# Performance work log

Measured on AMD Instinct MI355X. Metric: run time of the kernel, lower is better.

The kernel has to match this reference:

```python
import jax, jax.numpy as jnp
import numpy as np
import math, itertools

RANGE = 1.0
DIM = 3
N_LEVELS = 16
N_FEATS = 2
HASHMAP_SIZE = 2 ** 15
BASE_RES = 16
FINEST_RES = 512
_b = math.exp((math.log(FINEST_RES) - math.log(BASE_RES)) / (N_LEVELS - 1))
RESOLUTIONS = [int(math.floor(BASE_RES * (_b ** i))) for i in range(N_LEVELS)]
PRIMES = np.array([1, 2654435761, 805459861], dtype=np.uint32)
# True -> take the lower corner (xi) along that dim, weight (1 - xf)
BIN_MASK = np.array(list(itertools.product([1, 0], repeat=DIM)), dtype=bool)  # (8, 3)


def setup_inputs() -> dict:
    key = jax.random.key(0)
    kx, kt = jax.random.split(key)
    x = jax.random.uniform(kx, (1048576, DIM), jnp.float32, minval=-RANGE, maxval=RANGE)
    # per-level hash tables (nn.Embedding weights), stacked: (L, 2^15, F)
    tables = jax.random.normal(kt, (N_LEVELS, HASHMAP_SIZE, N_FEATS), jnp.float32) * 0.01
    return {"x": x, "tables": tables}


def _encode_level(x01, table, res):
    # x01: (N, 3) in [0, 1];  table: (2^15, F)
    xs = x01 * res
    xi_f = jnp.floor(xs)
    xf = (xs - xi_f)[:, None, :]                       # (N, 1, 3) fractional part
    xi = xi_f.astype(jnp.uint32)[:, None, :]           # (N, 1, 3)
    mask = jnp.asarray(BIN_MASK)[None]                 # (1, 8, 3)
    corners = jnp.where(mask, xi, xi + jnp.uint32(1))  # (N, 8, 3)
    ws = jnp.prod(jnp.where(mask, 1.0 - xf, xf), axis=-1)  # (N, 8) trilinear weights
    h = corners * jnp.asarray(PRIMES)                  # uint32 mul with wraparound
    idx = (h[..., 0] ^ h[..., 1] ^ h[..., 2]) % jnp.uint32(HASHMAP_SIZE)  # (N, 8)
    feats = table[idx]                                 # (N, 8, F) irregular gather
    return jnp.sum(feats * ws[..., None], axis=-2)     # (N, F)


def reference(x, tables):
    # HashGridLoRAEncoder.forward: normalize to [0,1], encode, concat levels
    x01 = (x + RANGE) / (2.0 * RANGE)                  # (N, 3)
    outs = [_encode_level(x01, tables[i], RESOLUTIONS[i]) for i in range(N_LEVELS)]
    return jnp.concatenate(outs, axis=-1)              # (N, 32)
```

## Files before the change

### kernel.cpp

```cpp
#include <hip/hip_runtime.h>

#define TMASK 32767u
#define P2 2654435761u
#define P3 805459861u

typedef float f32x4 __attribute__((ext_vector_type(4)));
typedef unsigned u32x4 __attribute__((ext_vector_type(4)));

constexpr int NBINS = 32768;
constexpr int BLOCK = 128;
constexpr int HP = 17;

constexpr size_t WS_HIST   = 0;
constexpr size_t WS_CURSOR = 128 * 1024;
constexpr size_t WS_SORTED = 256 * 1024;
constexpr size_t WS_NEEDED = WS_SORTED + (size_t)1048576 * 16;

__device__ __forceinline__ unsigned part1by2(unsigned v) {
    v &= 0x3FFu;
    v = (v | (v << 16)) & 0x030000FFu;
    v = (v | (v << 8))  & 0x0300F00Fu;
    v = (v | (v << 4))  & 0x030C30C3u;
    v = (v | (v << 2))  & 0x09249249u;
    return v;
}

__device__ __forceinline__ unsigned morton_key(float px, float py, float pz) {
    const float x01 = (px + 1.0f) * 0.5f;
    const float y01 = (py + 1.0f) * 0.5f;
    const float z01 = (pz + 1.0f) * 0.5f;
    const unsigned cx = min(31u, (unsigned)(x01 * 32.0f));
    const unsigned cy = min(31u, (unsigned)(y01 * 32.0f));
    const unsigned cz = min(31u, (unsigned)(z01 * 32.0f));
    return part1by2(cx) | (part1by2(cy) << 1) | (part1by2(cz) << 2);
}

__global__ void zero_hist_kernel(unsigned* __restrict__ hist) {
    const int i = blockIdx.x * blockDim.x + threadIdx.x;
    if (i < NBINS) hist[i] = 0u;
}

__global__ __launch_bounds__(256) void hist_kernel(const float* __restrict__ xin,
                                                   unsigned* __restrict__ hist, int n) {
    const int j = blockIdx.x * blockDim.x + threadIdx.x;
    const int p0 = j * 4;
    if (p0 + 3 < n) {
        const f32x4* xb = (const f32x4*)(xin + (size_t)p0 * 3);
        const f32x4 a = __builtin_nontemporal_load(xb + 0);
        const f32x4 b = __builtin_nontemporal_load(xb + 1);
        const f32x4 c = __builtin_nontemporal_load(xb + 2);
        atomicAdd(&hist[morton_key(a[0], a[1], a[2])], 1u);
        atomicAdd(&hist[morton_key(a[3], b[0], b[1])], 1u);
        atomicAdd(&hist[morton_key(b[2], b[3], c[0])], 1u);
        atomicAdd(&hist[morton_key(c[1], c[2], c[3])], 1u);
    } else {
        for (int p = p0; p < n; ++p) {
            const size_t bb = 3ull * (size_t)p;
            atomicAdd(&hist[morton_key(xin[bb], xin[bb + 1], xin[bb + 2])], 1u);
        }
    }
}

__global__ __launch_bounds__(1024) void scan_kernel(const unsigned* __restrict__ hist,
                                                    unsigned* __restrict__ cursor) {
    const int t = threadIdx.x;
    const u32x4* h4 = (const u32x4*)hist;
    u32x4 v[8];
    #pragma unroll
    for (int k = 0; k < 8; ++k) v[k] = h4[t * 8 + k];

    unsigned loc[32];
    unsigned s = 0;
    #pragma unroll
    for (int k = 0; k < 8; ++k) {
        loc[4 * k + 0] = s; s += v[k][0];
        loc[4 * k + 1] = s; s += v[k][1];
        loc[4 * k + 2] = s; s += v[k][2];
        loc[4 * k + 3] = s; s += v[k][3];
    }

    const int lane = t & 63;
    unsigned inc = s;
    #pragma unroll
    for (int off = 1; off < 64; off <<= 1) {
        const unsigned u = __shfl_up(inc, off, 64);
        if (lane >= off) inc += u;
    }

    __shared__ unsigned wtot[16];
    if (lane == 63) wtot[t >> 6] = inc;
    __syncthreads();
    if (t < 16) {
        unsigned w = wtot[t];
        const unsigned orig = w;
        #pragma unroll
        for (int off = 1; off < 16; off <<= 1) {
            const unsigned u = __shfl_up(w, off, 16);
            if (t >= off) w += u;
        }
        wtot[t] = w - orig;
    }
    __syncthreads();

    const unsigned base = wtot[t >> 6] + (inc - s);
    u32x4* c4 = (u32x4*)cursor;
    #pragma unroll
    for (int k = 0; k < 8; ++k) {
        u32x4 o = { base + loc[4 * k + 0], base + loc[4 * k + 1],
                    base + loc[4 * k + 2], base + loc[4 * k + 3] };
        c4[t * 8 + k] = o;
    }
}

__global__ __launch_bounds__(256) void scatter_kernel(const float* __restrict__ xin,
                                                      unsigned* __restrict__ cursor,
                                                      f32x4* __restrict__ sortedx, int n) {
    const int j = blockIdx.x * blockDim.x + threadIdx.x;
    const int p0 = j * 4;
    if (p0 + 3 < n) {
        const f32x4* xb = (const f32x4*)(xin + (size_t)p0 * 3);
        const f32x4 a = __builtin_nontemporal_load(xb + 0);
        const f32x4 b = __builtin_nontemporal_load(xb + 1);
        const f32x4 c = __builtin_nontemporal_load(xb + 2);
        const float X[4] = { a[0], a[3], b[2], c[1] };
        const float Y[4] = { a[1], b[0], b[3], c[2] };
        const float Z[4] = { a[2], b[1], c[0], c[3] };
        #pragma unroll
        for (int q = 0; q < 4; ++q) {
            const unsigned k = morton_key(X[q], Y[q], Z[q]);
            const unsigned slot = atomicAdd(&cursor[k], 1u);
            f32x4 v = { X[q], Y[q], Z[q], __uint_as_float((unsigned)(p0 + q)) };
            sortedx[slot] = v;
        }
    } else {
        for (int p = p0; p < n; ++p) {
            const size_t bb = 3ull * (size_t)p;
            const float px = xin[bb], py = xin[bb + 1], pz = xin[bb + 2];
            const unsigned k = morton_key(px, py, pz);
            const unsigned slot = atomicAdd(&cursor[k], 1u);
            f32x4 v = { px, py, pz, __uint_as_float((unsigned)p) };
            sortedx[slot] = v;
        }
    }
}

__global__ __launch_bounds__(BLOCK, 8) void hashgrid_kernel(
    const float* __restrict__ xin, const f32x4* __restrict__ sortedx,
    const float* __restrict__ tables, float* __restrict__ out, int n, int sorted)
{
    __shared__ float lds[BLOCK * HP];
    __shared__ unsigned sorig[BLOCK];
    const int t = threadIdx.x;
    const int base = blockIdx.x * BLOCK;
    const int i = base + t;

    float px = 0.f, py = 0.f, pz = 0.f;
    unsigned orig = (unsigned)i;
    if (i < n) {
        if (sorted) {
            const f32x4 v = sortedx[i];
            px = v[0]; py = v[1]; pz = v[2];
            orig = __float_as_uint(v[3]);
        } else {
            const size_t xb = 3ull * (size_t)i;
            px = xin[xb + 0]; py = xin[xb + 1]; pz = xin[xb + 2];
        }
    }
    sorig[t] = orig;

    const float x01 = (px + 1.0f) * 0.5f;
    const float y01 = (py + 1.0f) * 0.5f;
    const float z01 = (pz + 1.0f) * 0.5f;

    constexpr int RES[16] = {16, 20, 25, 32, 40, 50, 64, 80,
                             101, 128, 161, 203, 256, 322, 406, 512};

    const int nf4 = min(n - base, BLOCK) * 4;

    #pragma unroll
    for (int h = 0; h < 2; ++h) {
        #pragma unroll
        for (int lo = 0; lo < 8; ++lo) {
            const int l = h * 8 + lo;
            const float rf = (float)RES[l];
            const float xs = x01 * rf, ys = y01 * rf, zs = z01 * rf;
            const float fxs = floorf(xs), fys = floorf(ys), fzs = floorf(zs);
            const float tx = xs - fxs, ty = ys - fys, tz = zs - fzs;
            const unsigned xi = (unsigned)fxs;
            const unsigned yi = (unsigned)fys;
            const unsigned zi = (unsigned)fzs;

            const unsigned hx0 = xi & TMASK;
            const unsigned hym = yi * P2;
            const unsigned hy0 = hym & TMASK;
            const unsigned hy1 = (hym + P2) & TMASK;
            const unsigned hzm = zi * P3;
            const unsigned hz0 = hzm & TMASK;
            const unsigned hz1 = (hzm + P3) & TMASK;

            const float wx0 = 1.f - tx, wy0 = 1.f - ty, wz0 = 1.f - tz;
            const bool xeven = (xi & 1u) == 0u;
            const float* tbl = tables + (size_t)l * 65536ull;

            float a0 = 0.f, a1 = 0.f;
            #pragma unroll
            for (int p = 0; p < 4; ++p) {
                const unsigned m  = ((p & 1) ? hy1 : hy0) ^ ((p & 2) ? hz1 : hz0);
                const float  wyz  = ((p & 1) ? ty : wy0) * ((p & 2) ? tz : wz0);
                const unsigned idx0 = hx0 ^ m;
                const unsigned e    = idx0 & ~1u;
                const f32x4 q = *(const f32x4*)(tbl + 2u * e);
                const bool lo2 = (idx0 & 1u) == 0u;
                const float c0x = lo2 ? q[0] : q[2];
                const float c0y = lo2 ? q[1] : q[3];
                float c1x, c1y;
                if (xeven) {
                    c1x = lo2 ? q[2] : q[0];
                    c1y = lo2 ? q[3] : q[1];
                } else {
                    const unsigned idx1 = (hx0 + 1u) ^ m;
                    const float2 f = *(const float2*)(tbl + 2u * idx1);
                    c1x = f.x; c1y = f.y;
                }
                const float w0 = wyz * wx0;
                const float w1 = wyz * tx;
                a0 = fmaf(w0, c0x, fmaf(w1, c1x, a0));
                a1 = fmaf(w0, c0y, fmaf(w1, c1y, a1));
            }
            lds[t * HP + 2 * lo]     = a0;
            lds[t * HP + 2 * lo + 1] = a1;
        }

        __syncthreads();

        #pragma unroll
        for (int j = 0; j < 4; ++j) {
            const int g = j * BLOCK + t;
            if (g < nf4) {
                const int p = g >> 2;
                const int e = (g & 3) * 4;
                const float* s = &lds[p * HP + e];
                f32x4 v = { s[0], s[1], s[2], s[3] };
                __builtin_nontemporal_store(
                    v, (f32x4*)(out + (size_t)sorig[p] * 32ull + (size_t)(h * 16 + e)));
            }
        }
        __syncthreads();
    }
}

extern "C" void kernel_launch(void* const* d_in, const int* in_sizes, int n_in,
                              void* d_out, int out_size, void* d_ws, size_t ws_size,
                              hipStream_t stream) {
    const float* x      = (const float*)d_in[0];
    const float* tables = (const float*)d_in[1];
    float* out          = (float*)d_out;

    const int n = in_sizes[0] / 3;
    const int sorted = (ws_size >= WS_NEEDED) ? 1 : 0;

    f32x4* sortedx = (f32x4*)((char*)d_ws + WS_SORTED);

    if (sorted) {
        unsigned* hist   = (unsigned*)((char*)d_ws + WS_HIST);
        unsigned* cursor = (unsigned*)((char*)d_ws + WS_CURSOR);
        const int nq = (n + 3) / 4;
        hipLaunchKernelGGL(zero_hist_kernel, dim3(NBINS / 256), dim3(256), 0, stream, hist);
        hipLaunchKernelGGL(hist_kernel, dim3((nq + 255) / 256), dim3(256), 0, stream,
                           x, hist, n);
        hipLaunchKernelGGL(scan_kernel, dim3(1), dim3(1024), 0, stream, hist, cursor);
        hipLaunchKernelGGL(scatter_kernel, dim3((nq + 255) / 256), dim3(256), 0, stream,
                           x, cursor, sortedx, n);
    }

    hipLaunchKernelGGL(hashgrid_kernel, dim3((n + BLOCK - 1) / BLOCK), dim3(BLOCK), 0, stream,
                       x, sortedx, tables, out, n, sorted);
}
```

Baseline: 392.9 us.

## Sort via rank-from-histogram permutation instead of scattering full points

The histogram pass now keeps each point's atomic return value as its rank within its Morton bin and packs it with the key into a 32-bit word. The scatter pass then writes only a 4-byte permutation index using cursor+rank, with no second atomic pass and no re-read of x. The main kernel gathers coordinates from x through the permutation instead of reading a sorted 16-byte copy. The zeroing kernel becomes a memset. This cuts scatter traffic and atomics, at the cost of random 12-byte reads of x in the main kernel.

```diff
diff --git a/kernel.cpp b/kernel.cpp
--- a/kernel.cpp
+++ b/kernel.cpp
@@ -13,8 +13,9 @@
 
 constexpr size_t WS_HIST   = 0;
 constexpr size_t WS_CURSOR = 128 * 1024;
-constexpr size_t WS_SORTED = 256 * 1024;
-constexpr size_t WS_NEEDED = WS_SORTED + (size_t)1048576 * 16;
+constexpr size_t WS_KEYR   = 256 * 1024;
+constexpr size_t WS_PERM   = WS_KEYR + (size_t)1048576 * 4;
+constexpr size_t WS_NEEDED = WS_PERM + (size_t)1048576 * 4;
 
 __device__ __forceinline__ unsigned part1by2(unsigned v) {
     v &= 0x3FFu;
@@ -35,28 +36,33 @@
     return part1by2(cx) | (part1by2(cy) << 1) | (part1by2(cz) << 2);
 }
 
-__global__ void zero_hist_kernel(unsigned* __restrict__ hist) {
-    const int i = blockIdx.x * blockDim.x + threadIdx.x;
-    if (i < NBINS) hist[i] = 0u;
-}
-
 __global__ __launch_bounds__(256) void hist_kernel(const float* __restrict__ xin,
-                                                   unsigned* __restrict__ hist, int n) {
+                                                   unsigned* __restrict__ hist,
+                                                   unsigned* __restrict__ keyrank, int n) {
     const int j = blockIdx.x * blockDim.x + threadIdx.x;
     const int p0 = j * 4;
     if (p0 + 3 < n) {
         const f32x4* xb = (const f32x4*)(xin + (size_t)p0 * 3);
-        const f32x4 a = __builtin_nontemporal_load(xb + 0);
-        const f32x4 b = __builtin_nontemporal_load(xb + 1);
-        const f32x4 c = __builtin_nontemporal_load(xb + 2);
-        atomicAdd(&hist[morton_key(a[0], a[1], a[2])], 1u);
-        atomicAdd(&hist[morton_key(a[3], b[0], b[1])], 1u);
-        atomicAdd(&hist[morton_key(b[2], b[3], c[0])], 1u);
-        atomicAdd(&hist[morton_key(c[1], c[2], c[3])], 1u);
+        const f32x4 a = xb[0];
+        const f32x4 b = xb[1];
+        const f32x4 c = xb[2];
+        const unsigned k0 = morton_key(a[0], a[1], a[2]);
+        const unsigned k1 = morton_key(a[3], b[0], b[1]);
+        const unsigned k2 = morton_key(b[2], b[3], c[0]);
+        const unsigned k3 = morton_key(c[1], c[2], c[3]);
+        const unsigned r0 = atomicAdd(&hist[k0], 1u);
+        const unsigned r1 = atomicAdd(&hist[k1], 1u);
+        const unsigned r2 = atomicAdd(&hist[k2], 1u);
+        const unsigned r3 = atomicAdd(&hist[k3], 1u);
+        u32x4 kr = { (r0 << 15) | k0, (r1 << 15) | k1,
+                     (r2 << 15) | k2, (r3 << 15) | k3 };
+        *(u32x4*)(keyrank + p0) = kr;
     } else {
         for (int p = p0; p < n; ++p) {
             const size_t bb = 3ull * (size_t)p;
-            atomicAdd(&hist[morton_key(xin[bb], xin[bb + 1], xin[bb + 2])], 1u);
+            const unsigned k = morton_key(xin[bb], xin[bb + 1], xin[bb + 2]);
+            const unsigned r = atomicAdd(&hist[k], 1u);
+            keyrank[p] = (r << 15) | k;
         }
     }
 }
@@ -112,40 +118,29 @@
     }
 }
 
-__global__ __launch_bounds__(256) void scatter_kernel(const float* __restrict__ xin,
-                                                      unsigned* __restrict__ cursor,
-                                                      f32x4* __restrict__ sortedx, int n) {
+__global__ __launch_bounds__(256) void scatter_kernel(const unsigned* __restrict__ keyrank,
+                                                      const unsigned* __restrict__ cursor,
+                                                      unsigned* __restrict__ perm, int n) {
     const int j = blockIdx.x * blockDim.x + threadIdx.x;
     const int p0 = j * 4;
     if (p0 + 3 < n) {
-        const f32x4* xb = (const f32x4*)(xin + (size_t)p0 * 3);
-        const f32x4 a = __builtin_nontemporal_load(xb + 0);
-        const f32x4 b = __builtin_nontemporal_load(xb + 1);
-        const f32x4 c = __builtin_nontemporal_load(xb + 2);
-        const float X[4] = { a[0], a[3], b[2], c[1] };
-        const float Y[4] = { a[1], b[0], b[3], c[2] };
-        const float Z[4] = { a[2], b[1], c[0], c[3] };
+        const u32x4 kr = *(const u32x4*)(keyrank + p0);
         #pragma unroll
         for (int q = 0; q < 4; ++q) {
-            const unsigned k = morton_key(X[q], Y[q], Z[q]);
-            const unsigned slot = atomicAdd(&cursor[k], 1u);
-            f32x4 v = { X[q], Y[q], Z[q], __uint_as_float((unsigned)(p0 + q)) };
-            sortedx[slot] = v;
+            const unsigned key  = kr[q] & TMASK;
+            const unsigned rank = kr[q] >> 15;
+            perm[cursor[key] + rank] = (unsigned)(p0 + q);
         }
     } else {
         for (int p = p0; p < n; ++p) {
-            const size_t bb = 3ull * (size_t)p;
-            const float px = xin[bb], py = xin[bb + 1], pz = xin[bb + 2];
-            const unsigned k = morton_key(px, py, pz);
-            const unsigned slot = atomicAdd(&cursor[k], 1u);
-            f32x4 v = { px, py, pz, __uint_as_float((unsigned)p) };
-            sortedx[slot] = v;
+            const unsigned krv  = keyrank[p];
+            perm[cursor[krv & TMASK] + (krv >> 15)] = (unsigned)p;
         }
     }
 }
 
 __global__ __launch_bounds__(BLOCK, 8) void hashgrid_kernel(
-    const float* __restrict__ xin, const f32x4* __restrict__ sortedx,
+    const float* __restrict__ xin, const unsigned* __restrict__ perm,
     const float* __restrict__ tables, float* __restrict__ out, int n, int sorted)
 {
     __shared__ float lds[BLOCK * HP];
@@ -157,13 +152,13 @@
     float px = 0.f, py = 0.f, pz = 0.f;
     unsigned orig = (unsigned)i;
     if (i < n) {
-        if (sorted) {
-            const f32x4 v = sortedx[i];
+        if (sorted) orig = perm[i];
+        const size_t xb = 3ull * (size_t)orig;
+        if ((int)orig + 1 < n) {
+            const f32x4 v = *(const f32x4*)(xin + xb);
             px = v[0]; py = v[1]; pz = v[2];
-            orig = __float_as_uint(v[3]);
         } else {
-            const size_t xb = 3ull * (size_t)i;
-            px = xin[xb + 0]; py = xin[xb + 1]; pz = xin[xb + 2];
+            px = xin[xb]; py = xin[xb + 1]; pz = xin[xb + 2];
         }
     }
     sorig[t] = orig;
@@ -259,20 +254,21 @@
     const int n = in_sizes[0] / 3;
     const int sorted = (ws_size >= WS_NEEDED) ? 1 : 0;
 
-    f32x4* sortedx = (f32x4*)((char*)d_ws + WS_SORTED);
+    unsigned* perm = (unsigned*)((char*)d_ws + WS_PERM);
 
     if (sorted) {
-        unsigned* hist   = (unsigned*)((char*)d_ws + WS_HIST);
-        unsigned* cursor = (unsigned*)((char*)d_ws + WS_CURSOR);
+        unsigned* hist    = (unsigned*)((char*)d_ws + WS_HIST);
+        unsigned* cursor  = (unsigned*)((char*)d_ws + WS_CURSOR);
+        unsigned* keyrank = (unsigned*)((char*)d_ws + WS_KEYR);
         const int nq = (n + 3) / 4;
-        hipLaunchKernelGGL(zero_hist_kernel, dim3(NBINS / 256), dim3(256), 0, stream, hist);
+        hipMemsetAsync(hist, 0, NBINS * sizeof(unsigned), stream);
         hipLaunchKernelGGL(hist_kernel, dim3((nq + 255) / 256), dim3(256), 0, stream,
-                           x, hist, n);
+                           x, hist, keyrank, n);
         hipLaunchKernelGGL(scan_kernel, dim3(1), dim3(1024), 0, stream, hist, cursor);
         hipLaunchKernelGGL(scatter_kernel, dim3((nq + 255) / 256), dim3(256), 0, stream,
-                           x, cursor, sortedx, n);
+                           keyrank, cursor, perm, n);
     }
 
     hipLaunchKernelGGL(hashgrid_kernel, dim3((n + BLOCK - 1) / BLOCK), dim3(BLOCK), 0, stream,
-                       x, sortedx, tables, out, n, sorted);
-}
+                       x, perm, tables, out, n, sorted);
+}
```

Result: faster. 353.1 us (-10.1%).
